# Kernel tuning notes

Hardware: AMD Instinct MI355X
Metric: run time of the kernel (lower is better)

Reference implementation:

```python
import jax, jax.numpy as jnp
import numpy as np

N = 100000   # nodes
E = 1600000  # edges (avg degree 16)
D = 64       # input feature dim


def _lin(k, i, o):
    return (jax.random.normal(k, (i, o), jnp.float32) / np.float32(np.sqrt(i)))


def setup_inputs() -> dict:
    key = jax.random.key(0)
    ks = jax.random.split(key, 12)
    return {
        "x": jax.random.normal(ks[0], (N, D), jnp.float32),
        "edge_index": jax.random.randint(ks[1], (2, E), 0, N, dtype=jnp.int64),
        # layer 1: SAGEConv(64, 64, 'pool')
        "W1_pool": _lin(ks[2], 64, 64), "b1_pool": jnp.zeros((64,), jnp.float32),
        "W1_self": _lin(ks[3], 64, 64), "W1_neigh": _lin(ks[4], 64, 64),
        "b1": jnp.zeros((64,), jnp.float32),
        # layer 2: SAGEConv(64, 32, 'pool')
        "W2_pool": _lin(ks[5], 64, 64), "b2_pool": jnp.zeros((64,), jnp.float32),
        "W2_self": _lin(ks[6], 64, 32), "W2_neigh": _lin(ks[7], 64, 32),
        "b2": jnp.zeros((32,), jnp.float32),
        # layer 3: SAGEConv(32, 32, 'mean')
        "W3_self": _lin(ks[8], 32, 32), "W3_neigh": _lin(ks[9], 32, 32),
        "b3": jnp.zeros((32,), jnp.float32),
    }


def _sage_pool(x, src, dst, Wp, bp, Ws, Wn, b):
    # max-pool aggregator: transform all nodes once (cheaper than per-edge),
    # gather per-edge, segment-max into destination nodes.
    m = jax.nn.relu(x @ Wp + bp)[src]                      # [E, in]
    agg = jax.ops.segment_max(m, dst, num_segments=N)     # [N, in]
    agg = jnp.where(jnp.isfinite(agg), agg, jnp.float32(0.0))  # isolated nodes -> 0
    return x @ Ws + agg @ Wn + b


def _sage_mean(x, src, dst, Ws, Wn, b):
    s = jax.ops.segment_sum(x[src], dst, num_segments=N)   # [N, in]
    cnt = jax.ops.segment_sum(jnp.ones((src.shape[0],), jnp.float32), dst,
                              num_segments=N)
    agg = s / jnp.maximum(cnt, jnp.float32(1.0))[:, None]
    return x @ Ws + agg @ Wn + b


def reference(x, edge_index,
              W1_pool, b1_pool, W1_self, W1_neigh, b1,
              W2_pool, b2_pool, W2_self, W2_neigh, b2,
              W3_self, W3_neigh, b3):
    src, dst = edge_index[0], edge_index[1]
    h = jax.nn.relu(_sage_pool(x, src, dst, W1_pool, b1_pool, W1_self, W1_neigh, b1))
    h = _sage_pool(h, src, dst, W2_pool, b2_pool, W2_self, W2_neigh, b2)
    h = _sage_mean(h, src, dst, W3_self, W3_neigh, b3)
    return h
```

## Files before the change

kernel.cpp:

```cpp
#include <hip/hip_runtime.h>
#include <hip/hip_bf16.h>


typedef unsigned int uint;
typedef short short8 __attribute__((ext_vector_type(8)));
typedef float f32x4 __attribute__((ext_vector_type(4)));
typedef float f32x2 __attribute__((ext_vector_type(2)));
typedef unsigned short u16x8 __attribute__((ext_vector_type(8)));

__device__ __forceinline__ float bf2f(unsigned short h){
  return __uint_as_float(((uint)h) << 16);
}
__device__ __forceinline__ unsigned short f2bf(float f){
  uint u = __float_as_uint(f);
  u += 0x7fffu + ((u >> 16) & 1u);
  return (unsigned short)(u >> 16);
}
__device__ __forceinline__ float lo16(uint u){ return __uint_as_float(u << 16); }
__device__ __forceinline__ float hi16(uint u){ return __uint_as_float(u & 0xffff0000u); }

__device__ __forceinline__ uint4 pkmax4(uint4 a, uint4 b){
  u16x8 x = __builtin_bit_cast(u16x8, a);
  u16x8 y = __builtin_bit_cast(u16x8, b);
  return __builtin_bit_cast(uint4, __builtin_elementwise_max(x, y));
}
__device__ __forceinline__ uint4 shflx4(uint4 a, int off){
  uint4 r;
  r.x = (uint)__shfl_xor((int)a.x, off, 64);
  r.y = (uint)__shfl_xor((int)a.y, off, 64);
  r.z = (uint)__shfl_xor((int)a.z, off, 64);
  r.w = (uint)__shfl_xor((int)a.w, off, 64);
  return r;
}
__device__ __forceinline__ f32x2 b2lo(uint u){
  f32x2 r; r.x = lo16(u); r.y = hi16(u); return r;
}

struct WConv {
  const void* src[13];
  int n[13], isbias[13], Cs[13], K[13], off[13];
};

__global__ void conv_w(WConv wc, unsigned short* wtbase, float* bbase,
                       const unsigned short* x, const int* ei,
                       int* flags, int* ccur, int NB){
  __shared__ int sflags[2];
  int t = threadIdx.x;
  if (t < 64){
    int sane = 0;
    #pragma unroll
    for (int k = 0; k < 4; ++k){
      int e = (x[(t * 4 + k) * 2] >> 7) & 0xff;
      sane += (e >= 118 && e <= 134);
    }
    #pragma unroll
    for (int off = 32; off; off >>= 1) sane += __shfl_down(sane, off, 64);
    unsigned long long b = __ballot(ei[1 + 2 * t] != 0);
    if (t == 0){ sflags[0] = (sane >= 128); sflags[1] = (b == 0ull); }
  }
  __syncthreads();
  int isbf = sflags[0];
  if (blockIdx.x == 0){
    if (t == 0){ flags[0] = sflags[0]; flags[1] = sflags[1]; }
    for (int i = t; i < NB; i += 256) ccur[i] = 0;
  }
  int bt = blockIdx.x, n = wc.n[bt];
  if (wc.isbias[bt]){
    float* d = bbase + wc.off[bt];
    for (int i = t; i < n; i += 256)
      d[i] = isbf ? bf2f(((const unsigned short*)wc.src[bt])[i])
                  : ((const float*)wc.src[bt])[i];
  } else {
    unsigned short* d = wtbase + wc.off[bt];
    int Cs = wc.Cs[bt], K = wc.K[bt], Cm = (1 << Cs) - 1;
    for (int i = t; i < n; i += 256){
      int k = i >> Cs, c = i & Cm;
      unsigned short v = isbf ? ((const unsigned short*)wc.src[bt])[i]
                              : f2bf(((const float*)wc.src[bt])[i]);
      d[c * K + k] = v;
    }
  }
}

__device__ __forceinline__ void load_edge(const void* ei, int E, int is64, int e,
                                          int& s, int& d){
  if (is64){
    const long long* p = (const long long*)ei;
    s = (int)p[e]; d = (int)p[E + e];
  } else {
    const int* p = (const int*)ei;
    s = p[e]; d = p[E + e];
  }
}

__device__ __forceinline__ short8 ld_fragA_bf16(const unsigned short* A, int row,
                                                int K, int koff){
  return *(const short8*)(A + (size_t)row * K + koff);
}
__device__ __forceinline__ short8 ld_fragA_f32(const float* A, int row,
                                               int K, int koff){
  const float* q = A + (size_t)row * K + koff;
  float4 f0 = *(const float4*)q;
  float4 f1 = *(const float4*)(q + 4);
  short8 r;
  r[0] = (short)f2bf(f0.x); r[1] = (short)f2bf(f0.y);
  r[2] = (short)f2bf(f0.z); r[3] = (short)f2bf(f0.w);
  r[4] = (short)f2bf(f1.x); r[5] = (short)f2bf(f1.y);
  r[6] = (short)f2bf(f1.z); r[7] = (short)f2bf(f1.w);
  return r;
}
__device__ __forceinline__ unsigned short f2bf_relu(float f){
  return (unsigned short)(f2bf(fmaxf(f, 0.f)) & 0x7fff);
}

#define CSR_CE 8192

__device__ __forceinline__ void phase1_body(
    const void* __restrict__ ei, const int* __restrict__ flags,
    int* __restrict__ ccur, uint* __restrict__ pairs,
    int E, int N, int NB, int S, int CAP, int blk,
    uint* hist, uint* gbase)
{
  int t = threadIdx.x;
  uint dmask = (1u << S) - 1u;
  int is64 = flags[1];
  int e0 = blk * CSR_CE;
  for (int i = t; i < 1024; i += 256) hist[i] = 0;
  __syncthreads();
  #pragma unroll 4
  for (int it = 0; it < CSR_CE / 256; ++it){
    int e = e0 + it * 256 + t;
    if (e >= E) break;
    int s, d; load_edge(ei, E, is64, e, s, d);
    if ((unsigned)s >= (unsigned)N || (unsigned)d >= (unsigned)N) continue;
    atomicAdd(&hist[d >> S], 1u);
  }
  __syncthreads();
  for (int b = t; b < NB; b += 256){
    uint c = hist[b];
    if (c) gbase[b] = (uint)atomicAdd(&ccur[b], (int)c);
    hist[b] = 0;
  }
  __syncthreads();
  #pragma unroll 4
  for (int it = 0; it < CSR_CE / 256; ++it){
    int e = e0 + it * 256 + t;
    if (e >= E) break;
    int s, d; load_edge(ei, E, is64, e, s, d);
    if ((unsigned)s >= (unsigned)N || (unsigned)d >= (unsigned)N) continue;
    int b = d >> S;
    uint local = atomicAdd(&hist[b], 1u);
    uint pos = gbase[b] + local;
    if (pos >= (uint)CAP) pos = (uint)CAP - 1;
    pairs[(size_t)b * CAP + pos] = ((uint)s << S) | ((uint)d & dmask);
  }
}

template<int AMODE>
__device__ __forceinline__ void mm1_body(
    const void* __restrict__ Av, const unsigned short* __restrict__ WaT,
    const float* __restrict__ bias, const int* __restrict__ flags,
    unsigned short* __restrict__ out, int N, int blk)
{
  int wid = threadIdx.x >> 6, lane = threadIdx.x & 63;
  int n0 = blk * 32;
  int m = lane & 15, quad = lane >> 4, koq = quad * 8;
  int colbase = wid * 16;
  int rowc0 = min(n0 + m, N - 1);
  int rowc1 = min(n0 + 16 + m, N - 1);
  bool af32 = (AMODE == 2) && (flags[0] == 0);
  f32x4 a0 = {0.f,0.f,0.f,0.f}, a1 = {0.f,0.f,0.f,0.f};
  #pragma unroll
  for (int k0 = 0; k0 < 64; k0 += 32){
    short8 af0 = af32 ? ld_fragA_f32((const float*)Av, rowc0, 64, k0 + koq)
                      : ld_fragA_bf16((const unsigned short*)Av, rowc0, 64, k0 + koq);
    short8 af1 = af32 ? ld_fragA_f32((const float*)Av, rowc1, 64, k0 + koq)
                      : ld_fragA_bf16((const unsigned short*)Av, rowc1, 64, k0 + koq);
    short8 wf = *(const short8*)(WaT + (size_t)(colbase + m) * 64 + k0 + koq);
    a0 = __builtin_amdgcn_mfma_f32_16x16x32_bf16(af0, wf, a0, 0, 0, 0);
    a1 = __builtin_amdgcn_mfma_f32_16x16x32_bf16(af1, wf, a1, 0, 0, 0);
  }
  float bv = bias[colbase + m];
  #pragma unroll
  for (int r = 0; r < 4; ++r){
    int rl = quad * 4 + r;
    if (n0 + rl < N)
      out[(size_t)(n0 + rl) * 64 + colbase + m] = f2bf_relu(a0[r] + bv);
    if (n0 + 16 + rl < N)
      out[(size_t)(n0 + 16 + rl) * 64 + colbase + m] = f2bf_relu(a1[r] + bv);
  }
}

template<int AMODE>
__global__ __launch_bounds__(256) void phase1_mm1(
    const void* __restrict__ ei, const int* __restrict__ flags,
    int* __restrict__ ccur, uint* __restrict__ pairs,
    int E, int N, int NB, int S, int CAP, int nP,
    const void* __restrict__ x, const unsigned short* __restrict__ W1pT,
    const float* __restrict__ b1p, unsigned short* __restrict__ mbuf)
{
  __shared__ uint hist[1024];
  __shared__ uint gbase[1024];
  if ((int)blockIdx.x < nP)
    phase1_body(ei, flags, ccur, pairs, E, N, NB, S, CAP, blockIdx.x, hist, gbase);
  else
    mm1_body<AMODE>(x, W1pT, b1p, flags, mbuf, N, blockIdx.x - nP);
}

__global__ void csr_scan0(const int* __restrict__ ccur, int* __restrict__ cbase,
                          int* __restrict__ rowptrN, int NB, int CAP)
{
  __shared__ int sm[256];
  int t = threadIdx.x;
  int g = (NB + 255) / 256;
  int vb = t * g, v[4], s = 0;
  for (int k = 0; k < g; ++k){
    int i = vb + k; int x = (i < NB) ? min(ccur[i], CAP) : 0; v[k] = x; s += x;
  }
  sm[t] = s; __syncthreads();
  for (int off = 1; off < 256; off <<= 1){
    int x = (t >= off) ? sm[t - off] : 0;
    __syncthreads(); sm[t] += x; __syncthreads();
  }
  int run = sm[t] - s;
  for (int k = 0; k < g; ++k){
    int i = vb + k;
    if (i < NB){ cbase[i] = run; run += v[k]; }
  }
  if (t == 255){ cbase[NB] = run; *rowptrN = run; }
}

#define P2_CAP 6144
__global__ __launch_bounds__(256) void csr_phase2(
    const int* __restrict__ cbase, const int* __restrict__ ccur,
    const uint* __restrict__ pairs,
    int* __restrict__ bucket, int* __restrict__ row_ptr, int N, int S, int CAP)
{
  __shared__ int lbuf[P2_CAP];
  __shared__ int cur[1024];
  __shared__ int sm[256];
  int b = blockIdx.x, t = threadIdx.x;
  uint dmask = (1u << S) - 1u;
  int n0 = b << S;
  int n1 = n0 + (1 << S); if (n1 > N) n1 = N;
  int nn = n1 - n0;
  int base = cbase[b];
  int cnt = min(ccur[b], CAP);
  const uint* bp = pairs + (size_t)b * CAP;

  for (int i = t; i < nn; i += 256) cur[i] = 0;
  __syncthreads();
  for (int j = t; j < cnt; j += 256)
    atomicAdd(&cur[(int)(bp[j] & dmask)], 1);
  __syncthreads();
  int g = (nn + 255) / 256, vb = t * g, v[4], s = 0;
  for (int k = 0; k < g; ++k){
    int i = vb + k; int x = (i < nn) ? cur[i] : 0; v[k] = x; s += x;
  }
  sm[t] = s; __syncthreads();
  for (int off = 1; off < 256; off <<= 1){
    int x = (t >= off) ? sm[t - off] : 0;
    __syncthreads(); sm[t] += x; __syncthreads();
  }
  int run = sm[t] - s;
  for (int k = 0; k < g; ++k){
    int i = vb + k;
    if (i < nn){ row_ptr[n0 + i] = base + run; cur[i] = run; run += v[k]; }
  }
  __syncthreads();
  if (cnt <= 0) return;
  if (cnt <= P2_CAP){
    for (int j = t; j < cnt; j += 256){
      uint pr = bp[j];
      int pos = atomicAdd(&cur[(int)(pr & dmask)], 1);
      lbuf[pos] = (int)(pr >> S);
    }
    __syncthreads();
    for (int i = t; i < cnt; i += 256) bucket[base + i] = lbuf[i];
  } else {
    for (int j = t; j < cnt; j += 256){
      uint pr = bp[j];
      int pos = atomicAdd(&cur[(int)(pr & dmask)], 1);
      bucket[base + pos] = (int)(pr >> S);
    }
  }
}

__device__ __forceinline__ void gmax_pair(
    const int* __restrict__ row_ptr, const int* __restrict__ bucket,
    const unsigned short* __restrict__ m,
    unsigned short* la_row, int LDH, int nodeA, int N, int lane)
{
  int nodeB = nodeA + 1;
  int nAc = min(nodeA, N - 1);
  int rsA = row_ptr[nAc], reA = row_ptr[nAc + 1];
  int cntA = (nodeA < N) ? (reA - rsA) : 0;
  int rsB = reA;
  int cntB = (nodeB < N) ? (row_ptr[nodeB + 1] - reA) : 0;
  int fg8 = (lane & 7) * 8, rowsel = lane >> 3;
  uint4 accA = {0u,0u,0u,0u}, accB = {0u,0u,0u,0u};
  int cmax = max(cntA, cntB);
  for (int c0 = 0; c0 < cmax; c0 += 64){
    int chA = min(cntA - c0, 64);
    int chB = min(cntB - c0, 64);
    int bvA = (lane < chA) ? bucket[rsA + c0 + lane] : 0;
    int bvB = (lane < chB) ? bucket[rsB + c0 + lane] : 0;
    int it = (max(chA, chB) + 7) >> 3;
    for (int k = 0; k < it; ++k){
      int j = k * 8 + rowsel;
      int sA = __shfl(bvA, j, 64);
      int sB = __shfl(bvB, j, 64);
      uint4 vA = *(const uint4*)(m + (size_t)sA * 64 + fg8);
      uint4 vB = *(const uint4*)(m + (size_t)sB * 64 + fg8);
      if (j < chA) accA = pkmax4(accA, vA);
      if (j < chB) accB = pkmax4(accB, vB);
    }
  }
  #pragma unroll
  for (int off = 8; off <= 32; off <<= 1){
    accA = pkmax4(accA, shflx4(accA, off));
    accB = pkmax4(accB, shflx4(accB, off));
  }
  if (lane < 8){
    *(uint4*)(la_row + fg8) = accA;
  } else if (lane < 16){
    *(uint4*)(la_row + LDH + (lane & 7) * 8) = accB;
  }
}

template<int AMODE>
__global__ __launch_bounds__(256) void gmax_mm_fused(
    const void* __restrict__ Av, const unsigned short* __restrict__ msrc,
    const int* __restrict__ row_ptr, const int* __restrict__ bucket,
    const unsigned short* __restrict__ WaT, const unsigned short* __restrict__ WbT,
    const float* __restrict__ bias1,
    const unsigned short* __restrict__ WcT, const float* __restrict__ bias2,
    const int* __restrict__ flags,
    unsigned short* __restrict__ out1, unsigned short* __restrict__ out2, int N)
{
  constexpr int K = 64, C = 64, LDH = 72;
  __shared__ unsigned short la[32 * LDH];
  __shared__ unsigned short hl[32 * LDH];
  int wid = threadIdx.x >> 6, lane = threadIdx.x & 63;
  int n0 = blockIdx.x * 32;
  #pragma unroll
  for (int p = 0; p < 4; ++p){
    int lr = wid * 8 + p * 2;
    gmax_pair(row_ptr, bucket, msrc, la + (size_t)lr * LDH, LDH, n0 + lr, N, lane);
  }
  __syncthreads();
  int m = lane & 15, quad = lane >> 4, koq = quad * 8;
  int colbase = wid * 16;
  int rowc0 = min(n0 + m, N - 1);
  int rowc1 = min(n0 + 16 + m, N - 1);
  bool af32 = (AMODE == 2) && (flags[0] == 0);

  f32x4 a0 = {0.f,0.f,0.f,0.f}, a1 = {0.f,0.f,0.f,0.f};
  #pragma unroll
  for (int k0 = 0; k0 < K; k0 += 32){
    short8 af0 = af32 ? ld_fragA_f32((const float*)Av, rowc0, K, k0 + koq)
                      : ld_fragA_bf16((const unsigned short*)Av, rowc0, K, k0 + koq);
    short8 af1 = af32 ? ld_fragA_f32((const float*)Av, rowc1, K, k0 + koq)
                      : ld_fragA_bf16((const unsigned short*)Av, rowc1, K, k0 + koq);
    short8 wf = *(const short8*)(WaT + (size_t)(colbase + m) * K + k0 + koq);
    a0 = __builtin_amdgcn_mfma_f32_16x16x32_bf16(af0, wf, a0, 0, 0, 0);
    a1 = __builtin_amdgcn_mfma_f32_16x16x32_bf16(af1, wf, a1, 0, 0, 0);
    short8 bf0 = *(const short8*)(la + m * LDH + k0 + koq);
    short8 bf1 = *(const short8*)(la + (16 + m) * LDH + k0 + koq);
    short8 wg = *(const short8*)(WbT + (size_t)(colbase + m) * K + k0 + koq);
    a0 = __builtin_amdgcn_mfma_f32_16x16x32_bf16(bf0, wg, a0, 0, 0, 0);
    a1 = __builtin_amdgcn_mfma_f32_16x16x32_bf16(bf1, wg, a1, 0, 0, 0);
  }
  float bv = bias1[colbase + m];
  #pragma unroll
  for (int r = 0; r < 4; ++r){
    int rl = quad * 4 + r;
    unsigned short h0 = f2bf_relu(a0[r] + bv);
    unsigned short h1v = f2bf_relu(a1[r] + bv);
    hl[rl * LDH + colbase + m] = h0;
    hl[(16 + rl) * LDH + colbase + m] = h1v;
    if (n0 + rl < N) out1[(size_t)(n0 + rl) * C + colbase + m] = h0;
    if (n0 + 16 + rl < N) out1[(size_t)(n0 + 16 + rl) * C + colbase + m] = h1v;
  }
  __syncthreads();
  f32x4 c0 = {0.f,0.f,0.f,0.f}, c1 = {0.f,0.f,0.f,0.f};
  #pragma unroll
  for (int k0 = 0; k0 < K; k0 += 32){
    short8 q0 = *(const short8*)(hl + m * LDH + k0 + koq);
    short8 q1 = *(const short8*)(hl + (16 + m) * LDH + k0 + koq);
    short8 wf = *(const short8*)(WcT + (size_t)(colbase + m) * K + k0 + koq);
    c0 = __builtin_amdgcn_mfma_f32_16x16x32_bf16(q0, wf, c0, 0, 0, 0);
    c1 = __builtin_amdgcn_mfma_f32_16x16x32_bf16(q1, wf, c1, 0, 0, 0);
  }
  float b2v = bias2[colbase + m];
  #pragma unroll
  for (int r = 0; r < 4; ++r){
    int rl = quad * 4 + r;
    if (n0 + rl < N)
      out2[(size_t)(n0 + rl) * C + colbase + m] = f2bf_relu(c0[r] + b2v);
    if (n0 + 16 + rl < N)
      out2[(size_t)(n0 + 16 + rl) * C + colbase + m] = f2bf_relu(c1[r] + b2v);
  }
}

__global__ __launch_bounds__(256) void gmax_mm2(
    const unsigned short* __restrict__ h1, const unsigned short* __restrict__ msrc,
    const int* __restrict__ row_ptr, const int* __restrict__ bucket,
    const unsigned short* __restrict__ WsT, const unsigned short* __restrict__ WnT,
    const float* __restrict__ bias, unsigned short* __restrict__ h2, int N)
{
  constexpr int LDH = 72;
  __shared__ unsigned short la[64 * LDH];
  int wid = threadIdx.x >> 6, lane = threadIdx.x & 63;
  int n0 = blockIdx.x * 64;
  #pragma unroll
  for (int p = 0; p < 8; ++p){
    int lr = wid * 16 + p * 2;
    gmax_pair(row_ptr, bucket, msrc, la + (size_t)lr * LDH, LDH, n0 + lr, N, lane);
  }
  __syncthreads();
  int m = lane & 15, quad = lane >> 4, koq = quad * 8;
  int colbase = (wid & 1) * 16;
  int rb = (wid >> 1) * 32;
  int rowc0 = min(n0 + rb + m, N - 1), rowc1 = min(n0 + rb + 16 + m, N - 1);
  f32x4 a0 = {0.f,0.f,0.f,0.f}, a1 = {0.f,0.f,0.f,0.f};
  #pragma unroll
  for (int k0 = 0; k0 < 64; k0 += 32){
    short8 af0 = *(const short8*)(h1 + (size_t)rowc0 * 64 + k0 + koq);
    short8 af1 = *(const short8*)(h1 + (size_t)rowc1 * 64 + k0 + koq);
    short8 wf = *(const short8*)(WsT + (size_t)(colbase + m) * 64 + k0 + koq);
    a0 = __builtin_amdgcn_mfma_f32_16x16x32_bf16(af0, wf, a0, 0, 0, 0);
    a1 = __builtin_amdgcn_mfma_f32_16x16x32_bf16(af1, wf, a1, 0, 0, 0);
    short8 bf0 = *(const short8*)(la + (rb + m) * LDH + k0 + koq);
    short8 bf1 = *(const short8*)(la + (rb + 16 + m) * LDH + k0 + koq);
    short8 wg = *(const short8*)(WnT + (size_t)(colbase + m) * 64 + k0 + koq);
    a0 = __builtin_amdgcn_mfma_f32_16x16x32_bf16(bf0, wg, a0, 0, 0, 0);
    a1 = __builtin_amdgcn_mfma_f32_16x16x32_bf16(bf1, wg, a1, 0, 0, 0);
  }
  float bv = bias[colbase + m];
  #pragma unroll
  for (int r = 0; r < 4; ++r){
    int rl = quad * 4 + r;
    if (n0 + rb + rl < N)
      h2[(size_t)(n0 + rb + rl) * 32 + colbase + m] = f2bf(a0[r] + bv);
    if (n0 + rb + 16 + rl < N)
      h2[(size_t)(n0 + rb + 16 + rl) * 32 + colbase + m] = f2bf(a1[r] + bv);
  }
}

__global__ __launch_bounds__(256) void gsum3(
    const int* __restrict__ row_ptr, const int* __restrict__ bucket,
    const unsigned short* __restrict__ h2,
    const unsigned short* __restrict__ W3sT, const unsigned short* __restrict__ W3nT,
    const float* __restrict__ b3, float* __restrict__ out, int N)
{
  constexpr int LDA = 40;
  __shared__ unsigned short la[16 * LDA];
  int t = threadIdx.x;
  int w = t >> 6, lane = t & 63;
  int n0 = blockIdx.x * 16;
  int g = lane >> 4, q = lane & 15;
  int nd = n0 + w * 4 + g;
  int ndc = nd < N ? nd : N - 1;
  int rs = row_ptr[ndc];
  int cnt = (nd < N) ? (row_ptr[ndc + 1] - rs) : 0;
  int fg8 = (q & 3) * 8, rowsel = q >> 2;
  f32x2 a0 = {0.f,0.f}, a1 = {0.f,0.f}, a2 = {0.f,0.f}, a3 = {0.f,0.f};
  for (int c0 = 0; c0 < cnt; c0 += 16){
    int chunk = min(cnt - c0, 16);
    int bval = (q < chunk) ? bucket[rs + c0 + q] : 0;
    int it = (chunk + 3) >> 2;
    for (int k = 0; k < it; ++k){
      int j = k * 4 + rowsel;
      int s = __shfl(bval, (g << 4) + j, 64);
      uint4 v = *(const uint4*)(h2 + (size_t)s * 32 + fg8);
      if (j < chunk){
        a0 += b2lo(v.x); a1 += b2lo(v.y); a2 += b2lo(v.z); a3 += b2lo(v.w);
      }
    }
  }
  #pragma unroll
  for (int off = 4; off <= 8; off <<= 1){
    a0.x += __shfl_xor(a0.x, off, 64); a0.y += __shfl_xor(a0.y, off, 64);
    a1.x += __shfl_xor(a1.x, off, 64); a1.y += __shfl_xor(a1.y, off, 64);
    a2.x += __shfl_xor(a2.x, off, 64); a2.y += __shfl_xor(a2.y, off, 64);
    a3.x += __shfl_xor(a3.x, off, 64); a3.y += __shfl_xor(a3.y, off, 64);
  }
  if (rowsel == 0){
    float sc = 1.f / fmaxf((float)cnt, 1.f);
    int r = w * 4 + g;
    uint4 pk;
    pk.x = (uint)f2bf(a0.x * sc) | ((uint)f2bf(a0.y * sc) << 16);
    pk.y = (uint)f2bf(a1.x * sc) | ((uint)f2bf(a1.y * sc) << 16);
    pk.z = (uint)f2bf(a2.x * sc) | ((uint)f2bf(a2.y * sc) << 16);
    pk.w = (uint)f2bf(a3.x * sc) | ((uint)f2bf(a3.y * sc) << 16);
    *(uint4*)(la + r * LDA + q * 8) = pk;
  }
  __syncthreads();
  if (w < 2){
    int m = lane & 15, quad = lane >> 4, koq = quad * 8;
    int colbase = w * 16;
    int row = n0 + m;
    int rowc = row < N ? row : N - 1;
    f32x4 acc = {0.f, 0.f, 0.f, 0.f};
    short8 aself = *(const short8*)(h2 + (size_t)rowc * 32 + koq);
    short8 wfs = *(const short8*)(W3sT + (size_t)(colbase + m) * 32 + koq);
    acc = __builtin_amdgcn_mfma_f32_16x16x32_bf16(aself, wfs, acc, 0, 0, 0);
    short8 aagg = *(const short8*)(la + m * LDA + koq);
    short8 wfn = *(const short8*)(W3nT + (size_t)(colbase + m) * 32 + koq);
    acc = __builtin_amdgcn_mfma_f32_16x16x32_bf16(aagg, wfn, acc, 0, 0, 0);
    float bv = b3[colbase + m];
    #pragma unroll
    for (int r = 0; r < 4; ++r){
      int orow = n0 + quad * 4 + r;
      if (orow < N) out[(size_t)orow * 32 + colbase + m] = acc[r] + bv;
    }
  }
}

static inline char* align256(char* p){
  return (char*)(((uintptr_t)p + 255) & ~(uintptr_t)255);
}

extern "C" void kernel_launch(void* const* d_in, const int* in_sizes, int n_in,
                              void* d_out, int out_size, void* d_ws, size_t ws_size,
                              hipStream_t stream)
{
  const void* x = d_in[0];
  const void* ei = d_in[1];
  int N = in_sizes[0] / 64;
  int E = in_sizes[1] / 2;

  char* ws = (char*)d_ws;
  unsigned short* wtbase = (unsigned short*)ws;
  float* bbase = (float*)(ws + 65536);
  int* flags = (int*)(ws + 131072 - 256);

  int S = 7, NB = (N + 127) >> 7;
  while (NB > 1024){ S++; NB = (N + (1 << S) - 1) >> S; }
  int CAP = ((2 * E / NB) + 255) & ~255;
  if (CAP < 1024) CAP = 1024;

  char* p = ws + 131072;
  int* row_ptr = (int*)p; p = align256(p + (size_t)(N + 1) * 4);
  int* cbase   = (int*)p; p = align256(p + 4352);
  int* ccur    = (int*)p; p = align256(p + 4352);
  int* bucket  = (int*)p; p = align256(p + (size_t)E * 4);
  uint* pairs  = (uint*)p; p = align256(p + (size_t)NB * CAP * 4);
  char* P = p;  p = align256(p + (size_t)N * 64 * 2);
  char* Q = p;  p = align256(p + (size_t)N * 64 * 2);
  char* R = p;  p = align256(p + (size_t)N * 64 * 2);
  unsigned short* m1 = (unsigned short*)P;
  unsigned short* h2 = (unsigned short*)P;
  unsigned short* m2 = (unsigned short*)Q;
  unsigned short* h1 = (unsigned short*)R;

  WConv wc;
  {
    const int widx[13] = {2, 3, 4, 5, 6, 7, 8, 9, 10, 11, 12, 13, 14};
    const int isb[13]  = {0, 1, 0, 0, 1, 0, 1, 0, 0, 1, 0, 0, 1};
    const int Cs[13]   = {6, 0, 6, 6, 0, 6, 0, 5, 5, 0, 5, 5, 0};
    const int Kk[13]   = {64, 0, 64, 64, 0, 64, 0, 64, 64, 0, 32, 32, 0};
    const int off[13]  = {0, 0, 4096, 8192, 64, 12288, 128, 16384, 18432, 192,
                          20480, 21504, 224};
    for (int i = 0; i < 13; ++i){
      wc.src[i] = d_in[widx[i]]; wc.n[i] = in_sizes[widx[i]];
      wc.isbias[i] = isb[i]; wc.Cs[i] = Cs[i]; wc.K[i] = Kk[i]; wc.off[i] = off[i];
    }
  }
  hipLaunchKernelGGL(conv_w, dim3(13), dim3(256), 0, stream, wc, wtbase, bbase,
                     (const unsigned short*)x, (const int*)ei, flags, ccur, NB);
  unsigned short* W1pT = wtbase + 0;     unsigned short* W1sT = wtbase + 4096;
  unsigned short* W1nT = wtbase + 8192;  unsigned short* W2pT = wtbase + 12288;
  unsigned short* W2sT = wtbase + 16384; unsigned short* W2nT = wtbase + 18432;
  unsigned short* W3sT = wtbase + 20480; unsigned short* W3nT = wtbase + 21504;
  float* b1p = bbase + 0;  float* b1 = bbase + 64; float* b2p = bbase + 128;
  float* b2 = bbase + 192; float* b3 = bbase + 224;

  int nP = (E + CSR_CE - 1) / CSR_CE;
  int RT32 = (N + 31) / 32;
  int RT16 = (N + 15) / 16;

  phase1_mm1<2><<<nP + RT32, 256, 0, stream>>>(
      ei, flags, ccur, pairs, E, N, NB, S, CAP, nP, x, W1pT, b1p, m1);
  csr_scan0<<<1, 256, 0, stream>>>(ccur, cbase, row_ptr + N, NB, CAP);
  csr_phase2<<<NB, 256, 0, stream>>>(cbase, ccur, pairs, bucket, row_ptr, N, S, CAP);

  gmax_mm_fused<2><<<RT32,256,0,stream>>>(
      x, m1, row_ptr, bucket, W1sT, W1nT, b1, W2pT, b2p, flags, h1, m2, N);

  gmax_mm2<<<(N + 63) / 64,256,0,stream>>>(
      h1, m2, row_ptr, bucket, W2sT, W2nT, b2, h2, N);

  gsum3<<<RT16,256,0,stream>>>(row_ptr, bucket, h2, W3sT, W3nT, b3,
                               (float*)d_out, N);
}
```

Before: 274.3 us.

## Gather-max eight nodes per wave with per-lane neighbor loops

Replaces the paired-node gather-max, where the whole wave loaded neighbor indices, broadcast them with shuffles and finished with a cross-lane xor reduction, by a scheme that assigns eight lanes to each of eight nodes. Each lane walks its node's neighbor list directly, with four loads unrolled per step, and writes its own 8-column slice to shared memory, so no shuffles or cross-lane reduction are needed. This removes the shuffle traffic and the serial loop over node pairs and keeps more independent loads in flight. The cost is that lanes in a wave now diverge on degree imbalance, and neighbor indices are fetched redundantly by the eight lanes sharing a node.

```diff
diff --git a/kernel.cpp b/kernel.cpp
--- a/kernel.cpp
+++ b/kernel.cpp
@@ -23,14 +23,6 @@
   u16x8 x = __builtin_bit_cast(u16x8, a);
   u16x8 y = __builtin_bit_cast(u16x8, b);
   return __builtin_bit_cast(uint4, __builtin_elementwise_max(x, y));
-}
-__device__ __forceinline__ uint4 shflx4(uint4 a, int off){
-  uint4 r;
-  r.x = (uint)__shfl_xor((int)a.x, off, 64);
-  r.y = (uint)__shfl_xor((int)a.y, off, 64);
-  r.z = (uint)__shfl_xor((int)a.z, off, 64);
-  r.w = (uint)__shfl_xor((int)a.w, off, 64);
-  return r;
 }
 __device__ __forceinline__ f32x2 b2lo(uint u){
   f32x2 r; r.x = lo16(u); r.y = hi16(u); return r;
@@ -286,46 +278,37 @@
   }
 }
 
-__device__ __forceinline__ void gmax_pair(
+__device__ __forceinline__ void gmax_oct8(
     const int* __restrict__ row_ptr, const int* __restrict__ bucket,
     const unsigned short* __restrict__ m,
-    unsigned short* la_row, int LDH, int nodeA, int N, int lane)
-{
-  int nodeB = nodeA + 1;
-  int nAc = min(nodeA, N - 1);
-  int rsA = row_ptr[nAc], reA = row_ptr[nAc + 1];
-  int cntA = (nodeA < N) ? (reA - rsA) : 0;
-  int rsB = reA;
-  int cntB = (nodeB < N) ? (row_ptr[nodeB + 1] - reA) : 0;
-  int fg8 = (lane & 7) * 8, rowsel = lane >> 3;
-  uint4 accA = {0u,0u,0u,0u}, accB = {0u,0u,0u,0u};
-  int cmax = max(cntA, cntB);
-  for (int c0 = 0; c0 < cmax; c0 += 64){
-    int chA = min(cntA - c0, 64);
-    int chB = min(cntB - c0, 64);
-    int bvA = (lane < chA) ? bucket[rsA + c0 + lane] : 0;
-    int bvB = (lane < chB) ? bucket[rsB + c0 + lane] : 0;
-    int it = (max(chA, chB) + 7) >> 3;
-    for (int k = 0; k < it; ++k){
-      int j = k * 8 + rowsel;
-      int sA = __shfl(bvA, j, 64);
-      int sB = __shfl(bvB, j, 64);
-      uint4 vA = *(const uint4*)(m + (size_t)sA * 64 + fg8);
-      uint4 vB = *(const uint4*)(m + (size_t)sB * 64 + fg8);
-      if (j < chA) accA = pkmax4(accA, vA);
-      if (j < chB) accB = pkmax4(accB, vB);
-    }
-  }
-  #pragma unroll
-  for (int off = 8; off <= 32; off <<= 1){
-    accA = pkmax4(accA, shflx4(accA, off));
-    accB = pkmax4(accB, shflx4(accB, off));
-  }
-  if (lane < 8){
-    *(uint4*)(la_row + fg8) = accA;
-  } else if (lane < 16){
-    *(uint4*)(la_row + LDH + (lane & 7) * 8) = accB;
-  }
+    unsigned short* la_base, int LDH, int node0, int N, int lane)
+{
+  int ni = lane >> 3;
+  int col = (lane & 7) * 8;
+  int node = node0 + ni;
+  int nc = min(node, N - 1);
+  int rs = row_ptr[nc];
+  int re = row_ptr[nc + 1];
+  int cnt = (node < N) ? (re - rs) : 0;
+  uint4 acc = {0u, 0u, 0u, 0u};
+  int t = 0;
+  for (; t + 4 <= cnt; t += 4){
+    int s0 = bucket[rs + t];
+    int s1 = bucket[rs + t + 1];
+    int s2 = bucket[rs + t + 2];
+    int s3 = bucket[rs + t + 3];
+    uint4 v0 = *(const uint4*)(m + (size_t)s0 * 64 + col);
+    uint4 v1 = *(const uint4*)(m + (size_t)s1 * 64 + col);
+    uint4 v2 = *(const uint4*)(m + (size_t)s2 * 64 + col);
+    uint4 v3 = *(const uint4*)(m + (size_t)s3 * 64 + col);
+    acc = pkmax4(acc, pkmax4(pkmax4(v0, v1), pkmax4(v2, v3)));
+  }
+  for (; t < cnt; ++t){
+    int s = bucket[rs + t];
+    uint4 v = *(const uint4*)(m + (size_t)s * 64 + col);
+    acc = pkmax4(acc, v);
+  }
+  *(uint4*)(la_base + (size_t)ni * LDH + col) = acc;
 }
 
 template<int AMODE>
@@ -343,11 +326,8 @@
   __shared__ unsigned short hl[32 * LDH];
   int wid = threadIdx.x >> 6, lane = threadIdx.x & 63;
   int n0 = blockIdx.x * 32;
-  #pragma unroll
-  for (int p = 0; p < 4; ++p){
-    int lr = wid * 8 + p * 2;
-    gmax_pair(row_ptr, bucket, msrc, la + (size_t)lr * LDH, LDH, n0 + lr, N, lane);
-  }
+  gmax_oct8(row_ptr, bucket, msrc, la + (size_t)(wid * 8) * LDH, LDH,
+            n0 + wid * 8, N, lane);
   __syncthreads();
   int m = lane & 15, quad = lane >> 4, koq = quad * 8;
   int colbase = wid * 16;
@@ -413,11 +393,10 @@
   __shared__ unsigned short la[64 * LDH];
   int wid = threadIdx.x >> 6, lane = threadIdx.x & 63;
   int n0 = blockIdx.x * 64;
-  #pragma unroll
-  for (int p = 0; p < 8; ++p){
-    int lr = wid * 16 + p * 2;
-    gmax_pair(row_ptr, bucket, msrc, la + (size_t)lr * LDH, LDH, n0 + lr, N, lane);
-  }
+  gmax_oct8(row_ptr, bucket, msrc, la + (size_t)(wid * 16) * LDH, LDH,
+            n0 + wid * 16, N, lane);
+  gmax_oct8(row_ptr, bucket, msrc, la + (size_t)(wid * 16 + 8) * LDH, LDH,
+            n0 + wid * 16 + 8, N, lane);
   __syncthreads();
   int m = lane & 15, quad = lane >> 4, koq = quad * 8;
   int colbase = (wid & 1) * 16;
```

After: 274.1 us. Within noise of the previous version (-0.1%).
